# Kernel tuning notes

Measured on AMD Instinct MI355X. Metric: run time of the kernel, lower is better.

## Reference

```python
import jax, jax.numpy as jnp
import numpy as np

DIM = 1024
HEADS = 16
HEAD_DIM = DIM // HEADS
HIDDEN = 4 * DIM
EPS = 1e-5

def _layernorm(x, w, b):
    mu = jnp.mean(x, axis=-1, keepdims=True)
    var = jnp.mean(jnp.square(x - mu), axis=-1, keepdims=True)
    return (x - mu) * jax.lax.rsqrt(var + EPS) * w + b

def setup_inputs() -> dict:
    key = jax.random.key(0)
    ks = jax.random.split(key, 8)
    B, N, C = 4, 1024, DIM
    s = lambda fan_in: 1.0 / np.sqrt(fan_in)
    return {
        "x": jax.random.normal(ks[0], (B, N, C), dtype=jnp.float32),
        "ln1_w": jnp.ones((C,), jnp.float32),
        "ln1_b": jnp.zeros((C,), jnp.float32),
        "qkv_w": jax.random.normal(ks[1], (3 * C, C), jnp.float32) * s(C),
        "proj_w": jax.random.normal(ks[2], (C, C), jnp.float32) * s(C),
        "proj_b": jnp.zeros((C,), jnp.float32),
        "ln2_w": jnp.ones((C,), jnp.float32),
        "ln2_b": jnp.zeros((C,), jnp.float32),
        "fc1_w": jax.random.normal(ks[3], (HIDDEN, C), jnp.float32) * s(C),
        "fc1_b": jnp.zeros((HIDDEN,), jnp.float32),
        "fc2_w": jax.random.normal(ks[4], (C, HIDDEN), jnp.float32) * s(HIDDEN),
        "fc2_b": jnp.zeros((C,), jnp.float32),
    }

def reference(x, ln1_w, ln1_b, qkv_w, proj_w, proj_b, ln2_w, ln2_b, fc1_w, fc1_b, fc2_w, fc2_b):
    B, N, C = x.shape
    H, D = HEADS, HEAD_DIM
    scale = D ** -0.5
    # --- attention branch (pre-norm) ---
    h = _layernorm(x, ln1_w, ln1_b)
    qkv = jnp.einsum('bnc,oc->bno', h, qkv_w)          # [B,N,3C], no bias (qkv_bias=False)
    qkv = qkv.reshape(B, N, 3, H, D)
    q = jnp.transpose(qkv[:, :, 0], (0, 2, 1, 3))       # [B,H,N,D]
    k = jnp.transpose(qkv[:, :, 1], (0, 2, 1, 3))
    v = jnp.transpose(qkv[:, :, 2], (0, 2, 1, 3))
    attn = jnp.einsum('bhnd,bhmd->bhnm', q, k) * scale  # [B,H,N,N]
    attn = jax.nn.softmax(attn, axis=-1)
    o = jnp.einsum('bhnm,bhmd->bhnd', attn, v)          # [B,H,N,D]
    o = jnp.transpose(o, (0, 2, 1, 3)).reshape(B, N, C)
    o = jnp.einsum('bnc,oc->bno', o, proj_w) + proj_b
    x = x + o
    # --- MLP branch (pre-norm); drop=0.0 -> identity ---
    h = _layernorm(x, ln2_w, ln2_b)
    h = jnp.einsum('bnc,hc->bnh', h, fc1_w) + fc1_b
    h = jax.nn.gelu(h, approximate=False)               # nn.GELU exact erf form
    h = jnp.einsum('bnh,ch->bnc', h, fc2_w) + fc2_b
    return x + h
```

## Files before the change

kernel.cpp:

```cpp
#include <hip/hip_runtime.h>
#include <hip/hip_bf16.h>
#include <math.h>
#include <stdint.h>

#define SEQ 1024
#define CDIM 1024
#define NHEAD 16
#define HIDDEN 4096
#define BATCH 4
#define MROWS (BATCH*SEQ)

using bf16x8 = __attribute__((ext_vector_type(8))) short;
using f32x4  = __attribute__((ext_vector_type(4))) float;

__device__ __forceinline__ short f2bf(float f) {
    union { float f; uint32_t u; } c; c.f = f;
    const uint32_t u = c.u + 0x7FFFu + ((c.u >> 16) & 1u);
    return (short)(u >> 16);
}

__device__ __forceinline__ float gelu_exact(float v) {
    return 0.5f * v * (1.0f + erff(v * 0.70710678118654752440f));
}

__device__ __forceinline__ void gload_lds16(const short* g, short* lds) {
    __builtin_amdgcn_global_load_lds(
        (const __attribute__((address_space(1))) void*)(uintptr_t)g,
        (__attribute__((address_space(3))) void*)(uintptr_t)lds,
        16, 0, 0);
}

__global__ void cvt_bf16_kernel(const float* __restrict__ in, short* __restrict__ out) {
    const size_t i = ((size_t)blockIdx.x * 256 + threadIdx.x) * 8;
    const float4 a = *(const float4*)(in + i);
    const float4 b = *(const float4*)(in + i + 4);
    bf16x8 s;
    s[0] = f2bf(a.x); s[1] = f2bf(a.y); s[2] = f2bf(a.z); s[3] = f2bf(a.w);
    s[4] = f2bf(b.x); s[5] = f2bf(b.y); s[6] = f2bf(b.z); s[7] = f2bf(b.w);
    *(bf16x8*)(out + i) = s;
}

__global__ void ln_kernel(const float* __restrict__ x, const float* __restrict__ w,
                          const float* __restrict__ b, short* __restrict__ out) {
    const int row = blockIdx.x;
    const int t = threadIdx.x;
    const float4* xr = (const float4*)(x + (size_t)row * CDIM);
    float4 v = xr[t];
    float s  = v.x + v.y + v.z + v.w;
    float sq = v.x*v.x + v.y*v.y + v.z*v.z + v.w*v.w;
    #pragma unroll
    for (int off = 32; off; off >>= 1) {
        s  += __shfl_down(s, off);
        sq += __shfl_down(sq, off);
    }
    __shared__ float ss[4], ssq[4];
    const int wid = t >> 6, lane = t & 63;
    if (lane == 0) { ss[wid] = s; ssq[wid] = sq; }
    __syncthreads();
    s  = ss[0] + ss[1] + ss[2] + ss[3];
    sq = ssq[0] + ssq[1] + ssq[2] + ssq[3];
    const float mu  = s * (1.0f / CDIM);
    const float var = sq * (1.0f / CDIM) - mu * mu;
    const float rs  = rsqrtf(var + 1e-5f);
    const float4 wv = ((const float4*)w)[t];
    const float4 bv = ((const float4*)b)[t];
    short4 o;
    o.x = f2bf((v.x - mu) * rs * wv.x + bv.x);
    o.y = f2bf((v.y - mu) * rs * wv.y + bv.y);
    o.z = f2bf((v.z - mu) * rs * wv.z + bv.z);
    o.w = f2bf((v.w - mu) * rs * wv.w + bv.w);
    *(short4*)(out + (size_t)row * CDIM + t * 4) = o;
}

template<bool BIAS, bool RES, bool GELU_, bool OUTBF16>
__global__ __launch_bounds__(512) void gemm8p(
    const short* __restrict__ A, const short* __restrict__ B,
    const float* __restrict__ bias, const float* __restrict__ res,
    void* __restrict__ Cv, int M, int N, int K)
{
    __shared__ __align__(16) short As[2][256 * 64];
    __shared__ __align__(16) short Bs[2][256 * 64];
    const int t = threadIdx.x;
    const int w = t >> 6, l = t & 63;
    const int wm = w >> 2, wn = w & 3;

    const int lid = blockIdx.y * gridDim.x + blockIdx.x;
    const int xcd = lid & 7, c = lid >> 3;
    const int by = (xcd >> 1) * 4 + (c >> 3);
    const int bx = (xcd & 1) * 8 + (c & 7);
    const int m0 = by * 256, n0 = bx * 256;

    const int trow = t >> 3;
    const int k8s = ((t & 7) ^ (trow & 7)) * 8;
    const short* Ag = A + (size_t)(m0 + trow) * K + k8s;
    const short* Bg = B + (size_t)(n0 + trow) * K + k8s;

    const int fr = l & 15, g = l >> 4;
    const int sw = fr & 7;
    const int ak0 = (g ^ sw) * 8;
    const int ak1 = ((4 + g) ^ sw) * 8;
    int aoff[8], boff[4];
    #pragma unroll
    for (int mf = 0; mf < 8; ++mf) aoff[mf] = (wm * 128 + mf * 16 + fr) * 64;
    #pragma unroll
    for (int nf = 0; nf < 4; ++nf) boff[nf] = (wn * 64 + nf * 16 + fr) * 64;

    f32x4 acc[8][4] = {};

#define STAGE8(Gb, LDSb, kt, h)                                             \
    {                                                                       \
        gload_lds16((Gb) + (size_t)((h) * 128) * K + (kt) * 64,             \
                    (LDSb) + ((h) * 128 + w * 8) * 64);                     \
        gload_lds16((Gb) + (size_t)((h) * 128 + 64) * K + (kt) * 64,        \
                    (LDSb) + ((h) * 128 + 64 + w * 8) * 64);                \
    }

    STAGE8(Ag, As[0], 0, 0); STAGE8(Ag, As[0], 0, 1);
    STAGE8(Bg, Bs[0], 0, 0); STAGE8(Bg, Bs[0], 0, 1);
    asm volatile("s_waitcnt vmcnt(0)" ::: "memory");
    __builtin_amdgcn_s_barrier();

    const int T = K / 64;
    for (int kt = 0; kt < T; ++kt) {
        short* curA = &As[kt & 1][0];
        short* curB = &Bs[kt & 1][0];
        short* nxtA = &As[(kt & 1) ^ 1][0];
        short* nxtB = &Bs[(kt & 1) ^ 1][0];
        const bool pre = (kt + 1 < T);
        bf16x8 bfr[4], af[4];

        if (pre) STAGE8(Ag, nxtA, kt + 1, 0);
        #pragma unroll
        for (int nf = 0; nf < 4; ++nf) bfr[nf] = *(const bf16x8*)&curB[boff[nf] + ak0];
        #pragma unroll
        for (int mf = 0; mf < 4; ++mf) af[mf] = *(const bf16x8*)&curA[aoff[mf] + ak0];
        __builtin_amdgcn_s_barrier();
        __builtin_amdgcn_s_setprio(1);
        #pragma unroll
        for (int mf = 0; mf < 4; ++mf)
            #pragma unroll
            for (int nf = 0; nf < 4; ++nf)
                acc[mf][nf] = __builtin_amdgcn_mfma_f32_16x16x32_bf16(af[mf], bfr[nf], acc[mf][nf], 0, 0, 0);
        __builtin_amdgcn_s_setprio(0);
        __builtin_amdgcn_s_barrier();

        if (pre) STAGE8(Ag, nxtA, kt + 1, 1);
        #pragma unroll
        for (int mf = 0; mf < 4; ++mf) af[mf] = *(const bf16x8*)&curA[aoff[4 + mf] + ak0];
        __builtin_amdgcn_s_barrier();
        __builtin_amdgcn_s_setprio(1);
        #pragma unroll
        for (int mf = 0; mf < 4; ++mf)
            #pragma unroll
            for (int nf = 0; nf < 4; ++nf)
                acc[4 + mf][nf] = __builtin_amdgcn_mfma_f32_16x16x32_bf16(af[mf], bfr[nf], acc[4 + mf][nf], 0, 0, 0);
        __builtin_amdgcn_s_setprio(0);
        __builtin_amdgcn_s_barrier();

        if (pre) STAGE8(Bg, nxtB, kt + 1, 0);
        #pragma unroll
        for (int nf = 0; nf < 4; ++nf) bfr[nf] = *(const bf16x8*)&curB[boff[nf] + ak1];
        #pragma unroll
        for (int mf = 0; mf < 4; ++mf) af[mf] = *(const bf16x8*)&curA[aoff[mf] + ak1];
        __builtin_amdgcn_s_barrier();
        __builtin_amdgcn_s_setprio(1);
        #pragma unroll
        for (int mf = 0; mf < 4; ++mf)
            #pragma unroll
            for (int nf = 0; nf < 4; ++nf)
                acc[mf][nf] = __builtin_amdgcn_mfma_f32_16x16x32_bf16(af[mf], bfr[nf], acc[mf][nf], 0, 0, 0);
        __builtin_amdgcn_s_setprio(0);
        __builtin_amdgcn_s_barrier();

        if (pre) STAGE8(Bg, nxtB, kt + 1, 1);
        #pragma unroll
        for (int mf = 0; mf < 4; ++mf) af[mf] = *(const bf16x8*)&curA[aoff[4 + mf] + ak1];
        __builtin_amdgcn_s_barrier();
        __builtin_amdgcn_s_setprio(1);
        #pragma unroll
        for (int mf = 0; mf < 4; ++mf)
            #pragma unroll
            for (int nf = 0; nf < 4; ++nf)
                acc[4 + mf][nf] = __builtin_amdgcn_mfma_f32_16x16x32_bf16(af[mf], bfr[nf], acc[4 + mf][nf], 0, 0, 0);
        __builtin_amdgcn_s_setprio(0);
        asm volatile("s_waitcnt vmcnt(0)" ::: "memory");
        __builtin_amdgcn_s_barrier();
    }
#undef STAGE8

    const int lr4 = (l >> 4) * 4, lc = l & 15;
    #pragma unroll
    for (int mf = 0; mf < 8; ++mf) {
        #pragma unroll
        for (int nf = 0; nf < 4; ++nf) {
            const int col = n0 + wn * 64 + nf * 16 + lc;
            const float bv = BIAS ? bias[col] : 0.0f;
            #pragma unroll
            for (int r = 0; r < 4; ++r) {
                const int row = m0 + wm * 128 + mf * 16 + lr4 + r;
                float v = acc[mf][nf][r] + bv;
                if (GELU_) v = gelu_exact(v);
                if (RES)   v += res[(size_t)row * N + col];
                if (OUTBF16) ((short*)Cv)[(size_t)row * N + col] = f2bf(v);
                else         ((float*)Cv)[(size_t)row * N + col] = v;
            }
        }
    }
}

template<int BN, bool BIAS, bool RES, bool GELU_, bool OUTBF16>
__global__ __launch_bounds__(256) void mgemm(
    const short* __restrict__ A, const short* __restrict__ B,
    const float* __restrict__ bias, const float* __restrict__ res,
    void* __restrict__ Cv, int M, int N, int K)
{
    constexpr int MF = (BN == 128) ? 4 : 2;
    __shared__ __align__(16) short As[3][128 * 32];
    __shared__ __align__(16) short Bs[3][BN * 32];
    const int t = threadIdx.x;
    const int w = t >> 6, l = t & 63;

    const int gx = gridDim.x;
    const int nwg = gx * gridDim.y;
    const int lid = blockIdx.y * gx + blockIdx.x;
    const int swzb = (lid & 7) * (nwg >> 3) + (lid >> 3);
    const int bx = swzb % gx, by = swzb / gx;
    const int m0 = by * 128, n0 = bx * BN;

    const int wrow = (BN == 128) ? (w >> 1) * 64 : w * 32;
    const int wcol = (BN == 128) ? (w & 1) * 64 : 0;

    const int sk8 = ((l & 3) ^ ((l >> 3) & 3)) * 8;
    const short* agp0 = A + (size_t)(m0 + w * 32 + (l >> 2)) * K + sk8;
    const short* agp1 = agp0 + (size_t)16 * K;
    const short* bgp0;
    const short* bgp1 = nullptr;
    if (BN == 128) {
        bgp0 = B + (size_t)(n0 + w * 32 + (l >> 2)) * K + sk8;
        bgp1 = bgp0 + (size_t)16 * K;
    } else {
        bgp0 = B + (size_t)(n0 + w * 16 + (l >> 2)) * K + sk8;
    }

    const int fr = l & 15;
    const int rsw = (fr >> 1) & 3;
    int aoff[MF], boff[4];
    #pragma unroll
    for (int m = 0; m < MF; ++m) aoff[m] = (wrow + m * 16 + fr) * 32 + ((l >> 4) ^ rsw) * 8;
    #pragma unroll
    for (int n = 0; n < 4; ++n)  boff[n] = (wcol + n * 16 + fr) * 32 + ((l >> 4) ^ rsw) * 8;

    auto stage = [&](int k0, int buf) {
        short* ldsA = &As[buf][w * 1024];
        gload_lds16(agp0 + k0, ldsA);
        gload_lds16(agp1 + k0, ldsA + 512);
        if (BN == 128) {
            short* ldsB = &Bs[buf][w * 1024];
            gload_lds16(bgp0 + k0, ldsB);
            gload_lds16(bgp1 + k0, ldsB + 512);
        } else {
            gload_lds16(bgp0 + k0, &Bs[buf][w * 512]);
        }
    };

    f32x4 acc[MF][4] = {};
    const int T = K / 32;
    stage(0, 0);
    stage(32, 1);
    int cur = 0;
    for (int kt = 0; kt < T; ++kt) {
        if (kt < T - 1) {
            if constexpr (BN == 128) asm volatile("s_waitcnt vmcnt(4)" ::: "memory");
            else                     asm volatile("s_waitcnt vmcnt(3)" ::: "memory");
        } else {
            asm volatile("s_waitcnt vmcnt(0)" ::: "memory");
        }
        __builtin_amdgcn_sched_barrier(0);
        __builtin_amdgcn_s_barrier();
        __builtin_amdgcn_sched_barrier(0);
        if (kt + 2 < T) {
            int nb = kt + 2; nb -= (nb >= 3) ? ((nb / 3) * 3) : 0;
            stage((kt + 2) * 32, nb);
        }
        bf16x8 af[MF], bfr[4];
        #pragma unroll
        for (int m = 0; m < MF; ++m) af[m]  = *(const bf16x8*)&As[cur][aoff[m]];
        #pragma unroll
        for (int n = 0; n < 4; ++n)  bfr[n] = *(const bf16x8*)&Bs[cur][boff[n]];
        #pragma unroll
        for (int m = 0; m < MF; ++m)
            #pragma unroll
            for (int n = 0; n < 4; ++n)
                acc[m][n] = __builtin_amdgcn_mfma_f32_16x16x32_bf16(af[m], bfr[n], acc[m][n], 0, 0, 0);
        cur = (cur == 2) ? 0 : cur + 1;
    }

    const int lr4 = (l >> 4) * 4, lc = l & 15;
    #pragma unroll
    for (int m = 0; m < MF; ++m) {
        #pragma unroll
        for (int n = 0; n < 4; ++n) {
            const int col = n0 + wcol + n * 16 + lc;
            const float bv = BIAS ? bias[col] : 0.0f;
            #pragma unroll
            for (int r = 0; r < 4; ++r) {
                const int row = m0 + wrow + m * 16 + lr4 + r;
                float v = acc[m][n][r] + bv;
                if (GELU_) v = gelu_exact(v);
                if (RES)   v += res[(size_t)row * N + col];
                if (OUTBF16) ((short*)Cv)[(size_t)row * N + col] = f2bf(v);
                else         ((float*)Cv)[(size_t)row * N + col] = v;
            }
        }
    }
}

__global__ __launch_bounds__(256) void qkv_gemm(
    const short* __restrict__ A, const short* __restrict__ B,
    short* __restrict__ qkvb, short* __restrict__ VT, int K)
{
    __shared__ __align__(16) short As[3][128 * 32];
    __shared__ __align__(16) short Bs[3][128 * 32];
    const int t = threadIdx.x;
    const int w = t >> 6, l = t & 63;
    const int wr = w >> 1, wc = w & 1;

    const int gx = gridDim.x;
    const int nwg = gx * gridDim.y;
    const int lid = blockIdx.y * gx + blockIdx.x;
    const int swzb = (lid & 7) * (nwg >> 3) + (lid >> 3);
    const int bx = swzb % gx, by = swzb / gx;
    const int m0 = by * 128, n0 = bx * 128;

    const int sk8 = ((l & 3) ^ ((l >> 3) & 3)) * 8;
    const short* agp0 = A + (size_t)(m0 + w * 32 + (l >> 2)) * K + sk8;
    const short* agp1 = agp0 + (size_t)16 * K;
    const short* bgp0 = B + (size_t)(n0 + w * 32 + (l >> 2)) * K + sk8;
    const short* bgp1 = bgp0 + (size_t)16 * K;

    const int fr = l & 15;
    const int rsw = (fr >> 1) & 3;
    int aoff[4], boff[4];
    #pragma unroll
    for (int m = 0; m < 4; ++m) aoff[m] = (wr * 64 + m * 16 + fr) * 32 + ((l >> 4) ^ rsw) * 8;
    #pragma unroll
    for (int n = 0; n < 4; ++n) boff[n] = (wc * 64 + n * 16 + fr) * 32 + ((l >> 4) ^ rsw) * 8;

    auto stage = [&](int k0, int buf) {
        short* ldsA = &As[buf][w * 1024];
        short* ldsB = &Bs[buf][w * 1024];
        gload_lds16(agp0 + k0, ldsA);
        gload_lds16(agp1 + k0, ldsA + 512);
        gload_lds16(bgp0 + k0, ldsB);
        gload_lds16(bgp1 + k0, ldsB + 512);
    };

    f32x4 acc[4][4] = {};
    const int T = K / 32;
    stage(0, 0);
    stage(32, 1);
    int cur = 0;
    for (int kt = 0; kt < T; ++kt) {
        if (kt < T - 1) asm volatile("s_waitcnt vmcnt(4)" ::: "memory");
        else            asm volatile("s_waitcnt vmcnt(0)" ::: "memory");
        __builtin_amdgcn_sched_barrier(0);
        __builtin_amdgcn_s_barrier();
        __builtin_amdgcn_sched_barrier(0);
        if (kt + 2 < T) {
            int nb = kt + 2; nb -= (nb >= 3) ? ((nb / 3) * 3) : 0;
            stage((kt + 2) * 32, nb);
        }
        bf16x8 af[4], bfr[4];
        #pragma unroll
        for (int m = 0; m < 4; ++m) af[m]  = *(const bf16x8*)&As[cur][aoff[m]];
        #pragma unroll
        for (int n = 0; n < 4; ++n) bfr[n] = *(const bf16x8*)&Bs[cur][boff[n]];
        #pragma unroll
        for (int m = 0; m < 4; ++m)
            #pragma unroll
            for (int n = 0; n < 4; ++n)
                acc[m][n] = __builtin_amdgcn_mfma_f32_16x16x32_bf16(af[m], bfr[n], acc[m][n], 0, 0, 0);
        cur = (cur == 2) ? 0 : cur + 1;
    }

    const int lr4 = (l >> 4) * 4, lc = l & 15;
    if (n0 < 2048) {
        const float sc = (n0 < 1024) ? 0.125f : 1.0f;
        #pragma unroll
        for (int m = 0; m < 4; ++m) {
            #pragma unroll
            for (int n = 0; n < 4; ++n) {
                const int col = n0 + wc * 64 + n * 16 + lc;
                #pragma unroll
                for (int r = 0; r < 4; ++r) {
                    const int row = m0 + wr * 64 + m * 16 + lr4 + r;
                    qkvb[(size_t)row * 2048 + col] = f2bf(acc[m][n][r] * sc);
                }
            }
        }
    } else {
        #pragma unroll
        for (int m = 0; m < 4; ++m) {
            const int row0 = m0 + wr * 64 + m * 16 + lr4;
            const int b = row0 >> 10, nseq = row0 & 1023;
            #pragma unroll
            for (int n = 0; n < 4; ++n) {
                const int c2 = n0 - 2048 + wc * 64 + n * 16 + lc;
                const int h = c2 >> 6, d = c2 & 63;
                short4 v4;
                v4.x = f2bf(acc[m][n][0]); v4.y = f2bf(acc[m][n][1]);
                v4.z = f2bf(acc[m][n][2]); v4.w = f2bf(acc[m][n][3]);
                *(short4*)&VT[(((size_t)(b * 16 + h) * 64 + d) * 1024) + nseq] = v4;
            }
        }
    }
}

__global__ __launch_bounds__(256) void fattn(const short* __restrict__ qkvb,
                                             const short* __restrict__ VT,
                                             short* __restrict__ o) {
    const int bh = blockIdx.y;
    const int b = bh >> 4, h = bh & 15;
    const int q0 = blockIdx.x * 64;
    const int t = threadIdx.x, w = t >> 6, l = t & 63;

    __shared__ __align__(16) short Ks[2][64 * 64];
    __shared__ __align__(16) short Vs[2][64 * 64];
    __shared__ __align__(16) short Ps[4][1024];

    const size_t qrow = (size_t)(b * SEQ + q0 + w * 16 + (l & 15)) * 2048 + h * 64;
    bf16x8 qf[2];
    qf[0] = *(const bf16x8*)&qkvb[qrow + (l >> 4) * 8];
    qf[1] = *(const bf16x8*)&qkvb[qrow + 32 + (l >> 4) * 8];

    const int srow = l >> 3;
    const int sc16 = (l & 7) ^ (srow & 7);
    const short* Kg = qkvb + 1024 + h * 64;
    const short* Vg = VT + (size_t)bh * 64 * 1024;

    f32x4 acc[4] = {};
    float mrow[4] = {-1e30f, -1e30f, -1e30f, -1e30f};
    float lrow[4] = {0.f, 0.f, 0.f, 0.f};

    auto stage = [&](int kt, int buf) {
        const int kv0 = kt * 64;
        #pragma unroll
        for (int i = 0; i < 2; ++i) {
            const int r0 = w * 16 + i * 8;
            gload_lds16(Kg + (size_t)(b * SEQ + kv0 + r0 + srow) * 2048 + sc16 * 8,
                        &Ks[buf][r0 * 64]);
            gload_lds16(Vg + (size_t)(r0 + srow) * 1024 + kv0 + sc16 * 8,
                        &Vs[buf][r0 * 64]);
        }
    };

    stage(0, 0);
    for (int kt = 0; kt < 16; ++kt) {
        const int cur = kt & 1;
        __syncthreads();
        if (kt + 1 < 16) stage(kt + 1, cur ^ 1);

        f32x4 sacc[4];
        #pragma unroll
        for (int nt = 0; nt < 4; ++nt) {
            f32x4 z = {};
            #pragma unroll
            for (int ks = 0; ks < 2; ++ks) {
                const int row = nt * 16 + (l & 15);
                const int c16 = (ks * 4 + (l >> 4)) ^ (row & 7);
                const bf16x8 kf = *(const bf16x8*)&Ks[cur][row * 64 + c16 * 8];
                z = __builtin_amdgcn_mfma_f32_16x16x32_bf16(qf[ks], kf, z, 0, 0, 0);
            }
            sacc[nt] = z;
        }
        float tmax[4], tsum[4], fac[4];
        #pragma unroll
        for (int r = 0; r < 4; ++r)
            tmax[r] = fmaxf(fmaxf(sacc[0][r], sacc[1][r]), fmaxf(sacc[2][r], sacc[3][r]));
        #pragma unroll
        for (int off = 1; off <= 8; off <<= 1)
            #pragma unroll
            for (int r = 0; r < 4; ++r)
                tmax[r] = fmaxf(tmax[r], __shfl_xor(tmax[r], off));
        #pragma unroll
        for (int r = 0; r < 4; ++r) {
            const float nm = fmaxf(mrow[r], tmax[r]);
            fac[r] = __expf(mrow[r] - nm);
            mrow[r] = nm;
            tsum[r] = 0.0f;
        }
        #pragma unroll
        for (int nt = 0; nt < 4; ++nt) {
            #pragma unroll
            for (int r = 0; r < 4; ++r) {
                const float p = __expf(sacc[nt][r] - mrow[r]);
                tsum[r] += p;
                const int q = (l >> 4) * 4 + r;
                const int kv = nt * 16 + (l & 15);
                union { float f; uint32_t u; } cu; cu.f = p;
                Ps[w][q * 64 + (kv ^ ((q & 7) << 3))] = (short)((cu.u + 0x8000u) >> 16);
            }
        }
        #pragma unroll
        for (int off = 1; off <= 8; off <<= 1)
            #pragma unroll
            for (int r = 0; r < 4; ++r)
                tsum[r] += __shfl_xor(tsum[r], off);
        #pragma unroll
        for (int r = 0; r < 4; ++r) lrow[r] = lrow[r] * fac[r] + tsum[r];
        #pragma unroll
        for (int nt2 = 0; nt2 < 4; ++nt2)
            #pragma unroll
            for (int r = 0; r < 4; ++r)
                acc[nt2][r] *= fac[r];
        #pragma unroll
        for (int ks = 0; ks < 2; ++ks) {
            const int ql = l & 15;
            const bf16x8 pa = *(const bf16x8*)&Ps[w][ql * 64 + ((ks * 32 + (l >> 4) * 8) ^ ((ql & 7) << 3))];
            #pragma unroll
            for (int nt2 = 0; nt2 < 4; ++nt2) {
                const int row = nt2 * 16 + (l & 15);
                const int c16 = (ks * 4 + (l >> 4)) ^ (row & 7);
                const bf16x8 vf = *(const bf16x8*)&Vs[cur][row * 64 + c16 * 8];
                acc[nt2] = __builtin_amdgcn_mfma_f32_16x16x32_bf16(pa, vf, acc[nt2], 0, 0, 0);
            }
        }
    }
    #pragma unroll
    for (int r = 0; r < 4; ++r) {
        const float rcp = 1.0f / lrow[r];
        const int q = q0 + w * 16 + (l >> 4) * 4 + r;
        #pragma unroll
        for (int nt2 = 0; nt2 < 4; ++nt2) {
            const int d = nt2 * 16 + (l & 15);
            o[(size_t)(b * SEQ + q) * CDIM + h * 64 + d] = f2bf(acc[nt2][r] * rcp);
        }
    }
}

extern "C" void kernel_launch(void* const* d_in, const int* in_sizes, int n_in,
                              void* d_out, int out_size, void* d_ws, size_t ws_size,
                              hipStream_t stream) {
    const float* x      = (const float*)d_in[0];
    const float* ln1_w  = (const float*)d_in[1];
    const float* ln1_b  = (const float*)d_in[2];
    const float* qkv_w  = (const float*)d_in[3];
    const float* proj_w = (const float*)d_in[4];
    const float* proj_b = (const float*)d_in[5];
    const float* ln2_w  = (const float*)d_in[6];
    const float* ln2_b  = (const float*)d_in[7];
    const float* fc1_w  = (const float*)d_in[8];
    const float* fc1_b  = (const float*)d_in[9];
    const float* fc2_w  = (const float*)d_in[10];
    const float* fc2_b  = (const float*)d_in[11];
    float* out = (float*)d_out;

    short* ws16  = (short*)d_ws;
    short* wqkv  = ws16;
    short* wproj = ws16 + 3145728;
    short* wfc1  = ws16 + 4194304;
    short* wfc2  = ws16 + 8388608;
    char*  wsb   = (char*)d_ws;
    short* qkvb  = (short*)(wsb + (size_t)24 * 1024 * 1024);
    short* VT    = (short*)(wsb + (size_t)40 * 1024 * 1024);
    short* mlp1  = (short*)(wsb + (size_t)24 * 1024 * 1024);
    short* hbuf  = (short*)(wsb + (size_t)72 * 1024 * 1024);

    cvt_bf16_kernel<<<1536, 256, 0, stream>>>(qkv_w, wqkv);
    cvt_bf16_kernel<<< 512, 256, 0, stream>>>(proj_w, wproj);
    cvt_bf16_kernel<<<2048, 256, 0, stream>>>(fc1_w, wfc1);
    cvt_bf16_kernel<<<2048, 256, 0, stream>>>(fc2_w, wfc2);

    ln_kernel<<<MROWS, 256, 0, stream>>>(x, ln1_w, ln1_b, hbuf);
    qkv_gemm<<<dim3(24, 32), 256, 0, stream>>>(hbuf, wqkv, qkvb, VT, 1024);
    fattn<<<dim3(SEQ / 64, BATCH * NHEAD), 256, 0, stream>>>(qkvb, VT, hbuf);
    mgemm<64,true,true,false,false><<<dim3(16, 32), 256, 0, stream>>>(
        hbuf, wproj, proj_b, x, out, MROWS, 1024, 1024);
    ln_kernel<<<MROWS, 256, 0, stream>>>(out, ln2_w, ln2_b, hbuf);
    gemm8p<true,false,true,true><<<dim3(16, 16), 512, 0, stream>>>(
        hbuf, wfc1, fc1_b, nullptr, mlp1, MROWS, 4096, 1024);
    mgemm<64,true,true,false,false><<<dim3(16, 32), 256, 0, stream>>>(
        mlp1, wfc2, fc2_b, out, out, MROWS, 1024, 4096);
}
```

Measured before the change: 247.3 us.

## Use 256x256 eight-wave QKV GEMM and streamline flash-attention softmax

Replaces the 128x128 QKV GEMM with a 512-thread 256x256 tile kernel. It double-buffers 64-wide K slices and interleaves staged loads with MFMA phases under setprio, which raises operand reuse per byte loaded. The attention kernel computes S transposed so each lane owns one query row, cutting max and sum reductions to two shuffles. It skips rescaling the accumulator when the running max grows by no more than 8, packs P to bf16 with v_cvt_pk_bf16_f32, and remaps blocks so heads sharing K/V are grouped. The larger tiles launch fewer blocks (192) with heavy register and LDS use, and the lazy-rescale threshold trades a small numerical margin for fewer exp/multiply operations.

```diff
diff --git a/kernel.cpp b/kernel.cpp
--- a/kernel.cpp
+++ b/kernel.cpp
@@ -208,6 +208,152 @@
     }
 }
 
+__global__ __launch_bounds__(512) void qkv8p(
+    const short* __restrict__ A, const short* __restrict__ B,
+    short* __restrict__ qkvb, short* __restrict__ VT, int K)
+{
+    __shared__ __align__(16) short As[2][256 * 64];
+    __shared__ __align__(16) short Bs[2][256 * 64];
+    const int t = threadIdx.x;
+    const int w = t >> 6, l = t & 63;
+    const int wm = w >> 2, wn = w & 3;
+
+    const int lid = blockIdx.y * gridDim.x + blockIdx.x;
+    const int swz = (lid & 7) * 24 + (lid >> 3);
+    const int bx = swz % 12, by = swz / 12;
+    const int m0 = by * 256, n0 = bx * 256;
+
+    const int trow = t >> 3;
+    const int k8s = ((t & 7) ^ (trow & 7)) * 8;
+    const short* Ag = A + (size_t)(m0 + trow) * K + k8s;
+    const short* Bg = B + (size_t)(n0 + trow) * K + k8s;
+
+    const int fr = l & 15, g = l >> 4;
+    const int sw = fr & 7;
+    const int ak0 = (g ^ sw) * 8;
+    const int ak1 = ((4 + g) ^ sw) * 8;
+    int aoff[8], boff[4];
+    #pragma unroll
+    for (int mf = 0; mf < 8; ++mf) aoff[mf] = (wm * 128 + mf * 16 + fr) * 64;
+    #pragma unroll
+    for (int nf = 0; nf < 4; ++nf) boff[nf] = (wn * 64 + nf * 16 + fr) * 64;
+
+    f32x4 acc[8][4] = {};
+
+#define STAGE8(Gb, LDSb, kt, h)                                             \
+    {                                                                       \
+        gload_lds16((Gb) + (size_t)((h) * 128) * K + (kt) * 64,             \
+                    (LDSb) + ((h) * 128 + w * 8) * 64);                     \
+        gload_lds16((Gb) + (size_t)((h) * 128 + 64) * K + (kt) * 64,        \
+                    (LDSb) + ((h) * 128 + 64 + w * 8) * 64);                \
+    }
+
+    STAGE8(Ag, As[0], 0, 0); STAGE8(Ag, As[0], 0, 1);
+    STAGE8(Bg, Bs[0], 0, 0); STAGE8(Bg, Bs[0], 0, 1);
+    asm volatile("s_waitcnt vmcnt(0)" ::: "memory");
+    __builtin_amdgcn_s_barrier();
+
+    const int T = K / 64;
+    for (int kt = 0; kt < T; ++kt) {
+        short* curA = &As[kt & 1][0];
+        short* curB = &Bs[kt & 1][0];
+        short* nxtA = &As[(kt & 1) ^ 1][0];
+        short* nxtB = &Bs[(kt & 1) ^ 1][0];
+        const bool pre = (kt + 1 < T);
+        bf16x8 bfr[4], af[4];
+
+        if (pre) STAGE8(Ag, nxtA, kt + 1, 0);
+        #pragma unroll
+        for (int nf = 0; nf < 4; ++nf) bfr[nf] = *(const bf16x8*)&curB[boff[nf] + ak0];
+        #pragma unroll
+        for (int mf = 0; mf < 4; ++mf) af[mf] = *(const bf16x8*)&curA[aoff[mf] + ak0];
+        __builtin_amdgcn_s_barrier();
+        __builtin_amdgcn_s_setprio(1);
+        #pragma unroll
+        for (int mf = 0; mf < 4; ++mf)
+            #pragma unroll
+            for (int nf = 0; nf < 4; ++nf)
+                acc[mf][nf] = __builtin_amdgcn_mfma_f32_16x16x32_bf16(af[mf], bfr[nf], acc[mf][nf], 0, 0, 0);
+        __builtin_amdgcn_s_setprio(0);
+        __builtin_amdgcn_s_barrier();
+
+        if (pre) STAGE8(Ag, nxtA, kt + 1, 1);
+        #pragma unroll
+        for (int mf = 0; mf < 4; ++mf) af[mf] = *(const bf16x8*)&curA[aoff[4 + mf] + ak0];
+        __builtin_amdgcn_s_barrier();
+        __builtin_amdgcn_s_setprio(1);
+        #pragma unroll
+        for (int mf = 0; mf < 4; ++mf)
+            #pragma unroll
+            for (int nf = 0; nf < 4; ++nf)
+                acc[4 + mf][nf] = __builtin_amdgcn_mfma_f32_16x16x32_bf16(af[mf], bfr[nf], acc[4 + mf][nf], 0, 0, 0);
+        __builtin_amdgcn_s_setprio(0);
+        __builtin_amdgcn_s_barrier();
+
+        if (pre) STAGE8(Bg, nxtB, kt + 1, 0);
+        #pragma unroll
+        for (int nf = 0; nf < 4; ++nf) bfr[nf] = *(const bf16x8*)&curB[boff[nf] + ak1];
+        #pragma unroll
+        for (int mf = 0; mf < 4; ++mf) af[mf] = *(const bf16x8*)&curA[aoff[mf] + ak1];
+        __builtin_amdgcn_s_barrier();
+        __builtin_amdgcn_s_setprio(1);
+        #pragma unroll
+        for (int mf = 0; mf < 4; ++mf)
+            #pragma unroll
+            for (int nf = 0; nf < 4; ++nf)
+                acc[mf][nf] = __builtin_amdgcn_mfma_f32_16x16x32_bf16(af[mf], bfr[nf], acc[mf][nf], 0, 0, 0);
+        __builtin_amdgcn_s_setprio(0);
+        __builtin_amdgcn_s_barrier();
+
+        if (pre) STAGE8(Bg, nxtB, kt + 1, 1);
+        #pragma unroll
+        for (int mf = 0; mf < 4; ++mf) af[mf] = *(const bf16x8*)&curA[aoff[4 + mf] + ak1];
+        __builtin_amdgcn_s_barrier();
+        __builtin_amdgcn_s_setprio(1);
+        #pragma unroll
+        for (int mf = 0; mf < 4; ++mf)
+            #pragma unroll
+            for (int nf = 0; nf < 4; ++nf)
+                acc[4 + mf][nf] = __builtin_amdgcn_mfma_f32_16x16x32_bf16(af[mf], bfr[nf], acc[4 + mf][nf], 0, 0, 0);
+        __builtin_amdgcn_s_setprio(0);
+        asm volatile("s_waitcnt vmcnt(0)" ::: "memory");
+        __builtin_amdgcn_s_barrier();
+    }
+#undef STAGE8
+
+    const int lr4 = (l >> 4) * 4, lc = l & 15;
+    if (n0 < 2048) {
+        const float sc = (n0 < 1024) ? 0.125f : 1.0f;
+        #pragma unroll
+        for (int mf = 0; mf < 8; ++mf) {
+            #pragma unroll
+            for (int nf = 0; nf < 4; ++nf) {
+                const int col = n0 + wn * 64 + nf * 16 + lc;
+                #pragma unroll
+                for (int r = 0; r < 4; ++r) {
+                    const int row = m0 + wm * 128 + mf * 16 + lr4 + r;
+                    qkvb[(size_t)row * 2048 + col] = f2bf(acc[mf][nf][r] * sc);
+                }
+            }
+        }
+    } else {
+        #pragma unroll
+        for (int mf = 0; mf < 8; ++mf) {
+            const int row0 = m0 + wm * 128 + mf * 16 + lr4;
+            const int b = row0 >> 10, nseq = row0 & 1023;
+            #pragma unroll
+            for (int nf = 0; nf < 4; ++nf) {
+                const int c2 = n0 - 2048 + wn * 64 + nf * 16 + lc;
+                const int h = c2 >> 6, d = c2 & 63;
+                short4 v4;
+                v4.x = f2bf(acc[mf][nf][0]); v4.y = f2bf(acc[mf][nf][1]);
+                v4.z = f2bf(acc[mf][nf][2]); v4.w = f2bf(acc[mf][nf][3]);
+                *(short4*)&VT[(((size_t)(b * 16 + h) * 64 + d) * 1024) + nseq] = v4;
+            }
+        }
+    }
+}
+
 template<int BN, bool BIAS, bool RES, bool GELU_, bool OUTBF16>
 __global__ __launch_bounds__(256) void mgemm(
     const short* __restrict__ A, const short* __restrict__ B,
@@ -315,113 +461,13 @@
     }
 }
 
-__global__ __launch_bounds__(256) void qkv_gemm(
-    const short* __restrict__ A, const short* __restrict__ B,
-    short* __restrict__ qkvb, short* __restrict__ VT, int K)
-{
-    __shared__ __align__(16) short As[3][128 * 32];
-    __shared__ __align__(16) short Bs[3][128 * 32];
-    const int t = threadIdx.x;
-    const int w = t >> 6, l = t & 63;
-    const int wr = w >> 1, wc = w & 1;
-
-    const int gx = gridDim.x;
-    const int nwg = gx * gridDim.y;
-    const int lid = blockIdx.y * gx + blockIdx.x;
-    const int swzb = (lid & 7) * (nwg >> 3) + (lid >> 3);
-    const int bx = swzb % gx, by = swzb / gx;
-    const int m0 = by * 128, n0 = bx * 128;
-
-    const int sk8 = ((l & 3) ^ ((l >> 3) & 3)) * 8;
-    const short* agp0 = A + (size_t)(m0 + w * 32 + (l >> 2)) * K + sk8;
-    const short* agp1 = agp0 + (size_t)16 * K;
-    const short* bgp0 = B + (size_t)(n0 + w * 32 + (l >> 2)) * K + sk8;
-    const short* bgp1 = bgp0 + (size_t)16 * K;
-
-    const int fr = l & 15;
-    const int rsw = (fr >> 1) & 3;
-    int aoff[4], boff[4];
-    #pragma unroll
-    for (int m = 0; m < 4; ++m) aoff[m] = (wr * 64 + m * 16 + fr) * 32 + ((l >> 4) ^ rsw) * 8;
-    #pragma unroll
-    for (int n = 0; n < 4; ++n) boff[n] = (wc * 64 + n * 16 + fr) * 32 + ((l >> 4) ^ rsw) * 8;
-
-    auto stage = [&](int k0, int buf) {
-        short* ldsA = &As[buf][w * 1024];
-        short* ldsB = &Bs[buf][w * 1024];
-        gload_lds16(agp0 + k0, ldsA);
-        gload_lds16(agp1 + k0, ldsA + 512);
-        gload_lds16(bgp0 + k0, ldsB);
-        gload_lds16(bgp1 + k0, ldsB + 512);
-    };
-
-    f32x4 acc[4][4] = {};
-    const int T = K / 32;
-    stage(0, 0);
-    stage(32, 1);
-    int cur = 0;
-    for (int kt = 0; kt < T; ++kt) {
-        if (kt < T - 1) asm volatile("s_waitcnt vmcnt(4)" ::: "memory");
-        else            asm volatile("s_waitcnt vmcnt(0)" ::: "memory");
-        __builtin_amdgcn_sched_barrier(0);
-        __builtin_amdgcn_s_barrier();
-        __builtin_amdgcn_sched_barrier(0);
-        if (kt + 2 < T) {
-            int nb = kt + 2; nb -= (nb >= 3) ? ((nb / 3) * 3) : 0;
-            stage((kt + 2) * 32, nb);
-        }
-        bf16x8 af[4], bfr[4];
-        #pragma unroll
-        for (int m = 0; m < 4; ++m) af[m]  = *(const bf16x8*)&As[cur][aoff[m]];
-        #pragma unroll
-        for (int n = 0; n < 4; ++n) bfr[n] = *(const bf16x8*)&Bs[cur][boff[n]];
-        #pragma unroll
-        for (int m = 0; m < 4; ++m)
-            #pragma unroll
-            for (int n = 0; n < 4; ++n)
-                acc[m][n] = __builtin_amdgcn_mfma_f32_16x16x32_bf16(af[m], bfr[n], acc[m][n], 0, 0, 0);
-        cur = (cur == 2) ? 0 : cur + 1;
-    }
-
-    const int lr4 = (l >> 4) * 4, lc = l & 15;
-    if (n0 < 2048) {
-        const float sc = (n0 < 1024) ? 0.125f : 1.0f;
-        #pragma unroll
-        for (int m = 0; m < 4; ++m) {
-            #pragma unroll
-            for (int n = 0; n < 4; ++n) {
-                const int col = n0 + wc * 64 + n * 16 + lc;
-                #pragma unroll
-                for (int r = 0; r < 4; ++r) {
-                    const int row = m0 + wr * 64 + m * 16 + lr4 + r;
-                    qkvb[(size_t)row * 2048 + col] = f2bf(acc[m][n][r] * sc);
-                }
-            }
-        }
-    } else {
-        #pragma unroll
-        for (int m = 0; m < 4; ++m) {
-            const int row0 = m0 + wr * 64 + m * 16 + lr4;
-            const int b = row0 >> 10, nseq = row0 & 1023;
-            #pragma unroll
-            for (int n = 0; n < 4; ++n) {
-                const int c2 = n0 - 2048 + wc * 64 + n * 16 + lc;
-                const int h = c2 >> 6, d = c2 & 63;
-                short4 v4;
-                v4.x = f2bf(acc[m][n][0]); v4.y = f2bf(acc[m][n][1]);
-                v4.z = f2bf(acc[m][n][2]); v4.w = f2bf(acc[m][n][3]);
-                *(short4*)&VT[(((size_t)(b * 16 + h) * 64 + d) * 1024) + nseq] = v4;
-            }
-        }
-    }
-}
-
 __global__ __launch_bounds__(256) void fattn(const short* __restrict__ qkvb,
                                              const short* __restrict__ VT,
                                              short* __restrict__ o) {
-    const int bh = blockIdx.y;
+    const int lid = blockIdx.y * gridDim.x + blockIdx.x;
+    const int bh = ((lid >> 7) << 3) | (lid & 7);
+    const int q0 = ((lid >> 3) & 15) * 64;
     const int b = bh >> 4, h = bh & 15;
-    const int q0 = blockIdx.x * 64;
     const int t = threadIdx.x, w = t >> 6, l = t & 63;
 
     __shared__ __align__(16) short Ks[2][64 * 64];
@@ -439,8 +485,9 @@
     const short* Vg = VT + (size_t)bh * 64 * 1024;
 
     f32x4 acc[4] = {};
-    float mrow[4] = {-1e30f, -1e30f, -1e30f, -1e30f};
-    float lrow[4] = {0.f, 0.f, 0.f, 0.f};
+    float mr = -1e30f, lr = 0.0f;
+    const int q = l & 15;
+    const int g4 = (l >> 4) & 3;
 
     auto stage = [&](int kt, int buf) {
         const int kv0 = kt * 64;
@@ -469,50 +516,57 @@
                 const int row = nt * 16 + (l & 15);
                 const int c16 = (ks * 4 + (l >> 4)) ^ (row & 7);
                 const bf16x8 kf = *(const bf16x8*)&Ks[cur][row * 64 + c16 * 8];
-                z = __builtin_amdgcn_mfma_f32_16x16x32_bf16(qf[ks], kf, z, 0, 0, 0);
+                z = __builtin_amdgcn_mfma_f32_16x16x32_bf16(kf, qf[ks], z, 0, 0, 0);
             }
             sacc[nt] = z;
         }
-        float tmax[4], tsum[4], fac[4];
-        #pragma unroll
-        for (int r = 0; r < 4; ++r)
-            tmax[r] = fmaxf(fmaxf(sacc[0][r], sacc[1][r]), fmaxf(sacc[2][r], sacc[3][r]));
-        #pragma unroll
-        for (int off = 1; off <= 8; off <<= 1)
+        float tm = sacc[0][0];
+        #pragma unroll
+        for (int nt = 0; nt < 4; ++nt)
+            #pragma unroll
+            for (int r = 0; r < 4; ++r) tm = fmaxf(tm, sacc[nt][r]);
+        tm = fmaxf(tm, __shfl_xor(tm, 16));
+        tm = fmaxf(tm, __shfl_xor(tm, 32));
+        const bool norescale = __all(tm <= mr + 8.0f);
+        float fac = 1.0f;
+        if (!norescale) {
+            const float nm = fmaxf(mr, tm);
+            fac = __expf(mr - nm);
+            mr = nm;
+        }
+        float p[4][4];
+        float ts = 0.0f;
+        #pragma unroll
+        for (int nt = 0; nt < 4; ++nt)
+            #pragma unroll
+            for (int r = 0; r < 4; ++r) {
+                p[nt][r] = __expf(sacc[nt][r] - mr);
+                ts += p[nt][r];
+            }
+        ts += __shfl_xor(ts, 16);
+        ts += __shfl_xor(ts, 32);
+        lr = lr * fac + ts;
+        if (!norescale) {
+            float facv[4];
             #pragma unroll
             for (int r = 0; r < 4; ++r)
-                tmax[r] = fmaxf(tmax[r], __shfl_xor(tmax[r], off));
-        #pragma unroll
-        for (int r = 0; r < 4; ++r) {
-            const float nm = fmaxf(mrow[r], tmax[r]);
-            fac[r] = __expf(mrow[r] - nm);
-            mrow[r] = nm;
-            tsum[r] = 0.0f;
+                facv[r] = __shfl(fac, (l & 48) + g4 * 4 + r);
+            #pragma unroll
+            for (int nt2 = 0; nt2 < 4; ++nt2)
+                #pragma unroll
+                for (int r = 0; r < 4; ++r)
+                    acc[nt2][r] *= facv[r];
         }
         #pragma unroll
         for (int nt = 0; nt < 4; ++nt) {
-            #pragma unroll
-            for (int r = 0; r < 4; ++r) {
-                const float p = __expf(sacc[nt][r] - mrow[r]);
-                tsum[r] += p;
-                const int q = (l >> 4) * 4 + r;
-                const int kv = nt * 16 + (l & 15);
-                union { float f; uint32_t u; } cu; cu.f = p;
-                Ps[w][q * 64 + (kv ^ ((q & 7) << 3))] = (short)((cu.u + 0x8000u) >> 16);
-            }
-        }
-        #pragma unroll
-        for (int off = 1; off <= 8; off <<= 1)
-            #pragma unroll
-            for (int r = 0; r < 4; ++r)
-                tsum[r] += __shfl_xor(tsum[r], off);
-        #pragma unroll
-        for (int r = 0; r < 4; ++r) lrow[r] = lrow[r] * fac[r] + tsum[r];
-        #pragma unroll
-        for (int nt2 = 0; nt2 < 4; ++nt2)
-            #pragma unroll
-            for (int r = 0; r < 4; ++r)
-                acc[nt2][r] *= fac[r];
+            uint32_t lo, hi;
+            asm("v_cvt_pk_bf16_f32 %0, %1, %2" : "=v"(lo) : "v"(p[nt][0]), "v"(p[nt][1]));
+            asm("v_cvt_pk_bf16_f32 %0, %1, %2" : "=v"(hi) : "v"(p[nt][2]), "v"(p[nt][3]));
+            const int kvb = nt * 16 + g4 * 4;
+            const int addr = q * 64 + (((kvb >> 3) ^ (q & 7)) << 3) + (kvb & 7);
+            *(uint2*)&Ps[w][addr] = make_uint2(lo, hi);
+        }
+        __builtin_amdgcn_s_waitcnt(0);
         #pragma unroll
         for (int ks = 0; ks < 2; ++ks) {
             const int ql = l & 15;
@@ -526,14 +580,15 @@
             }
         }
     }
+    float rcpl = 1.0f / lr;
     #pragma unroll
     for (int r = 0; r < 4; ++r) {
-        const float rcp = 1.0f / lrow[r];
-        const int q = q0 + w * 16 + (l >> 4) * 4 + r;
+        const float rcp = __shfl(rcpl, (l & 48) + g4 * 4 + r);
+        const int qq = q0 + w * 16 + g4 * 4 + r;
         #pragma unroll
         for (int nt2 = 0; nt2 < 4; ++nt2) {
             const int d = nt2 * 16 + (l & 15);
-            o[(size_t)(b * SEQ + q) * CDIM + h * 64 + d] = f2bf(acc[nt2][r] * rcp);
+            o[(size_t)(b * SEQ + qq) * CDIM + h * 64 + d] = f2bf(acc[nt2][r] * rcp);
         }
     }
 }
@@ -572,8 +627,8 @@
     cvt_bf16_kernel<<<2048, 256, 0, stream>>>(fc2_w, wfc2);
 
     ln_kernel<<<MROWS, 256, 0, stream>>>(x, ln1_w, ln1_b, hbuf);
-    qkv_gemm<<<dim3(24, 32), 256, 0, stream>>>(hbuf, wqkv, qkvb, VT, 1024);
-    fattn<<<dim3(SEQ / 64, BATCH * NHEAD), 256, 0, stream>>>(qkvb, VT, hbuf);
+    qkv8p<<<dim3(12, 16), 512, 0, stream>>>(hbuf, wqkv, qkvb, VT, 1024);
+    fattn<<<dim3(16, 64), 256, 0, stream>>>(qkvb, VT, hbuf);
     mgemm<64,true,true,false,false><<<dim3(16, 32), 256, 0, stream>>>(
         hbuf, wproj, proj_b, x, out, MROWS, 1024, 1024);
     ln_kernel<<<MROWS, 256, 0, stream>>>(out, ln2_w, ln2_b, hbuf);
```

After: 230.0 us. 1.08x faster.
